# Kernel optimization log

Hardware: AMD Instinct MI355X
Metric: run time of the kernel (lower is better)

The kernel has to match this reference:

```python
import jax, jax.numpy as jnp
import numpy as np

C = 192
NUM_HEADS = 4
K = 3
KV_STRIDE = 2
EPS = 1e-5


def _conv(x, w, stride, groups):
    # x: [B,C,H,W], w: [O, I//groups, kh, kw]
    return jax.lax.conv_general_dilated(
        x, w, window_strides=(stride, stride),
        padding=[(K // 2, K // 2), (K // 2, K // 2)] if w.shape[-1] > 1 else [(0, 0), (0, 0)],
        dimension_numbers=("NCHW", "OIHW", "NCHW"),
        feature_group_count=groups)


def _bn(x, gamma, beta, mean, var):
    # eval-mode batchnorm over channel dim of NCHW
    inv = gamma / jnp.sqrt(var + EPS)
    return x * inv[None, :, None, None] + (beta - mean * inv)[None, :, None, None]


def _dwconv_flatten(x, dw, g, b, m, v, pw, stride):
    y = _conv(x, dw, stride, groups=C)          # depthwise
    y = _bn(y, g, b, m, v)
    y = _conv(y, pw, 1, groups=1)               # 1x1 pointwise
    B, O, h, w = y.shape
    return y.reshape(B, O, h * w).transpose(0, 2, 1)  # b (h w) c


def setup_inputs() -> dict:
    key = jax.random.key(0)
    ks = jax.random.split(key, 16)
    B, H, W = 8, 56, 56
    d = {
        "x": jax.random.normal(ks[0], (B, H * W, C), jnp.float32),
        "H": H,
        "W": W,
        "dw_q": jax.random.normal(ks[1], (C, 1, K, K), jnp.float32) * 0.1,
        "bn_q_gamma": jax.random.uniform(ks[2], (C,), jnp.float32, 0.5, 1.5),
        "bn_q_beta": jax.random.normal(ks[3], (C,), jnp.float32) * 0.1,
        "bn_q_mean": jax.random.normal(ks[4], (C,), jnp.float32) * 0.1,
        "bn_q_var": jax.random.uniform(ks[5], (C,), jnp.float32, 0.5, 1.5),
        "pw_q": jax.random.normal(ks[6], (C, C, 1, 1), jnp.float32) * (1.0 / np.sqrt(C)),
        "dw_kv": jax.random.normal(ks[7], (C, 1, K, K), jnp.float32) * 0.1,
        "bn_kv_gamma": jax.random.uniform(ks[8], (C,), jnp.float32, 0.5, 1.5),
        "bn_kv_beta": jax.random.normal(ks[9], (C,), jnp.float32) * 0.1,
        "bn_kv_mean": jax.random.normal(ks[10], (C,), jnp.float32) * 0.1,
        "bn_kv_var": jax.random.uniform(ks[11], (C,), jnp.float32, 0.5, 1.5),
        "pw_kv": jax.random.normal(ks[12], (2 * C, C, 1, 1), jnp.float32) * (1.0 / np.sqrt(C)),
        "Wq": jax.random.normal(ks[13], (C, C), jnp.float32) * (1.0 / np.sqrt(C)),
        "bq": jnp.zeros((C,), jnp.float32),
        "Wk": jax.random.normal(ks[14], (C, C), jnp.float32) * (1.0 / np.sqrt(C)),
        "bk": jnp.zeros((C,), jnp.float32),
        "Wv": jax.random.normal(ks[15], (C, C), jnp.float32) * (1.0 / np.sqrt(C)),
        "bv": jnp.zeros((C,), jnp.float32),
    }
    return d


def reference(x, H, W, dw_q, bn_q_gamma, bn_q_beta, bn_q_mean, bn_q_var, pw_q,
              dw_kv, bn_kv_gamma, bn_kv_beta, bn_kv_mean, bn_kv_var, pw_kv,
              Wq, bq, Wk, bk, Wv, bv):
    B, N, _ = x.shape
    h = NUM_HEADS
    hd = C // h
    scale = hd ** -0.5
    # Token2Patch: b (H W) c -> b c H W
    xp = x.transpose(0, 2, 1).reshape(B, C, H, W)
    conv_q = _dwconv_flatten(xp, dw_q, bn_q_gamma, bn_q_beta, bn_q_mean, bn_q_var, pw_q, 1)  # [B,N,C]
    kv = _dwconv_flatten(xp, dw_kv, bn_kv_gamma, bn_kv_beta, bn_kv_mean, bn_kv_var, pw_kv, KV_STRIDE)  # [B,M,2C]
    conv_k, conv_v = kv[..., :C], kv[..., C:]
    q = (conv_q @ Wq.T + bq).reshape(B, N, h, hd).transpose(0, 2, 1, 3)      # [B,h,N,hd]
    M = conv_k.shape[1]
    k = (conv_k @ Wk.T + bk).reshape(B, M, h, hd).transpose(0, 2, 1, 3)      # [B,h,M,hd]
    v = (conv_v @ Wv.T + bv).reshape(B, M, h, hd).transpose(0, 2, 1, 3)      # [B,h,M,hd]
    attn = jnp.einsum("bhnd,bhmd->bhnm", q, k) * scale
    attn = jax.nn.softmax(attn, axis=-1)
    out = jnp.einsum("bhnm,bhmd->bhnd", attn, v)
    # MergeHeads: b h n d -> b n (h d)
    return out.transpose(0, 2, 1, 3).reshape(B, N, C)
```

## Files before the change

kernel.cpp:

```cpp
#include <hip/hip_runtime.h>
#include <cmath>

typedef _Float16 f16;
typedef _Float16 f16x8 __attribute__((ext_vector_type(8)));
typedef _Float16 f16x4 __attribute__((ext_vector_type(4)));
typedef float    f32x4 __attribute__((ext_vector_type(4)));
typedef unsigned int u32;
typedef u32 u32x2 __attribute__((ext_vector_type(2)));

#define C_   192
#define HH   56
#define WW   56
#define NN   3136
#define BB   8
#define MM   784
#define NHEAD 4
#define HD   48
#define VT_LD 832
#define KVPB (BB*MM/32)

#define MFMA16(a,b,c)  __builtin_amdgcn_mfma_f32_16x16x32_f16(a,b,c,0,0,0)
#define MFMAK16(a,b,c) __builtin_amdgcn_mfma_f32_16x16x16f16(a,b,c,0,0,0)

static __device__ __forceinline__ u32 pkrtz(float a, float b) {
    typedef __fp16 fp16x2 __attribute__((ext_vector_type(2)));
    fp16x2 h = __builtin_amdgcn_cvt_pkrtz(a, b);
    return __builtin_bit_cast(u32, h);
}

static __device__ __forceinline__ void gload16(const void* g, void* l) {
    __builtin_amdgcn_global_load_lds(
        (const __attribute__((address_space(1))) unsigned int*)g,
        (__attribute__((address_space(3))) unsigned int*)l, 16, 0, 0);
}

template<int STRIDE, int OH, int OW>
__device__ __forceinline__ void dwbn_quad(
    const float* __restrict__ x, const float* __restrict__ dwL,
    const float* __restrict__ gamma, const float* __restrict__ beta,
    const float* __restrict__ mean,  const float* __restrict__ var,
    f16* __restrict__ out, int idx)
{
    int c4 = idx % 48;
    int r1 = idx / 48;
    int qx = r1 % (OW/2);
    int r2 = r1 / (OW/2);
    int qp = r2 % (OH/2);
    int b  = r2 / (OH/2);
    int c0 = c4*4;

    float4 w4[9];
    #pragma unroll
    for (int j = 0; j < 9; ++j)
        w4[j] = *(const float4*)&dwL[c4*40 + j*4];
    const float* wf = (const float*)w4;

    float4 g4  = *(const float4*)(gamma + c0);
    float4 be4 = *(const float4*)(beta + c0);
    float4 m4  = *(const float4*)(mean + c0);
    float4 v4  = *(const float4*)(var  + c0);

    float4 a00 = make_float4(0.f,0.f,0.f,0.f);
    float4 a01 = a00, a10 = a00, a11 = a00;
    int iyTop = (2*qp)*STRIDE - 1;
    int ix0   = (2*qx)*STRIDE - 1;
    #pragma unroll
    for (int j = 0; j < STRIDE+3; ++j) {
        int iy = iyTop + j;
        if (iy < 0 || iy >= HH) continue;
        #pragma unroll
        for (int i = 0; i < STRIDE+3; ++i) {
            int ix = ix0 + i;
            if (ix < 0 || ix >= WW) continue;
            float4 xv = *reinterpret_cast<const float4*>(
                x + ((size_t)b*NN + iy*WW + ix)*C_ + c0);
            const bool r0ok = (j <= 2), r1ok = (j >= STRIDE);
            const bool c0ok = (i <= 2), c1ok = (i >= STRIDE);
            if (r0ok && c0ok) { const int wi = j*3 + i;
                a00.x = fmaf(wf[ 0+wi], xv.x, a00.x);
                a00.y = fmaf(wf[ 9+wi], xv.y, a00.y);
                a00.z = fmaf(wf[18+wi], xv.z, a00.z);
                a00.w = fmaf(wf[27+wi], xv.w, a00.w); }
            if (r0ok && c1ok) { const int wi = j*3 + (i-STRIDE);
                a01.x = fmaf(wf[ 0+wi], xv.x, a01.x);
                a01.y = fmaf(wf[ 9+wi], xv.y, a01.y);
                a01.z = fmaf(wf[18+wi], xv.z, a01.z);
                a01.w = fmaf(wf[27+wi], xv.w, a01.w); }
            if (r1ok && c0ok) { const int wi = (j-STRIDE)*3 + i;
                a10.x = fmaf(wf[ 0+wi], xv.x, a10.x);
                a10.y = fmaf(wf[ 9+wi], xv.y, a10.y);
                a10.z = fmaf(wf[18+wi], xv.z, a10.z);
                a10.w = fmaf(wf[27+wi], xv.w, a10.w); }
            if (r1ok && c1ok) { const int wi = (j-STRIDE)*3 + (i-STRIDE);
                a11.x = fmaf(wf[ 0+wi], xv.x, a11.x);
                a11.y = fmaf(wf[ 9+wi], xv.y, a11.y);
                a11.z = fmaf(wf[18+wi], xv.z, a11.z);
                a11.w = fmaf(wf[27+wi], xv.w, a11.w); }
        }
    }
    float i0 = g4.x*__frsqrt_rn(v4.x + 1e-5f);
    float i1 = g4.y*__frsqrt_rn(v4.y + 1e-5f);
    float i2 = g4.z*__frsqrt_rn(v4.z + 1e-5f);
    float i3 = g4.w*__frsqrt_rn(v4.w + 1e-5f);
    float b0 = be4.x - m4.x*i0, b1 = be4.y - m4.y*i1;
    float b2 = be4.z - m4.z*i2, b3 = be4.w - m4.w*i3;
    size_t base = (((size_t)b*OH + 2*qp)*OW + 2*qx)*48 + c4;
    f16x4 r;
    r[0]=(f16)(a00.x*i0+b0); r[1]=(f16)(a00.y*i1+b1);
    r[2]=(f16)(a00.z*i2+b2); r[3]=(f16)(a00.w*i3+b3);
    *reinterpret_cast<f16x4*>(out + base*4) = r;
    r[0]=(f16)(a01.x*i0+b0); r[1]=(f16)(a01.y*i1+b1);
    r[2]=(f16)(a01.z*i2+b2); r[3]=(f16)(a01.w*i3+b3);
    *reinterpret_cast<f16x4*>(out + (base + 48)*4) = r;
    r[0]=(f16)(a10.x*i0+b0); r[1]=(f16)(a10.y*i1+b1);
    r[2]=(f16)(a10.z*i2+b2); r[3]=(f16)(a10.w*i3+b3);
    *reinterpret_cast<f16x4*>(out + (base + (size_t)OW*48)*4) = r;
    r[0]=(f16)(a11.x*i0+b0); r[1]=(f16)(a11.y*i1+b1);
    r[2]=(f16)(a11.z*i2+b2); r[3]=(f16)(a11.w*i3+b3);
    *reinterpret_cast<f16x4*>(out + (base + (size_t)OW*48 + 48)*4) = r;
}

__global__ __launch_bounds__(256) void prep_all(
    const float* __restrict__ x,
    const float* __restrict__ dwq,  const float* __restrict__ gq,
    const float* __restrict__ bq_,  const float* __restrict__ mq,
    const float* __restrict__ vq,
    const float* __restrict__ dwkv, const float* __restrict__ gkv,
    const float* __restrict__ bkv,  const float* __restrict__ mkv,
    const float* __restrict__ vkv,
    const float* __restrict__ Wq, const float* __restrict__ Wk,
    const float* __restrict__ Wv, const float* __restrict__ pw_q,
    const float* __restrict__ pw_kv,
    f16* __restrict__ uq, f16* __restrict__ ukv,
    f16* __restrict__ Mq, f16* __restrict__ Mk, f16* __restrict__ Mv,
    f16* __restrict__ vt)
{
    int blk = blockIdx.x, tid = threadIdx.x;
    const int QB = 1176, KB = 294;
    if (blk < QB + KB) {
        bool qp = blk < QB;
        __shared__ __align__(16) float dwL[48*40];
        const float* dwg = qp ? dwq : dwkv;
        for (int i = tid; i < 432; i += 256) {
            int f  = i*4;
            int c4 = f/36, r = f%36;
            *(float4*)&dwL[c4*40 + r] = *(const float4*)(dwg + f);
        }
        __syncthreads();
        if (qp)
            dwbn_quad<1, HH, WW>(x, dwL, gq, bq_, mq, vq, uq, blk*256 + tid);
        else
            dwbn_quad<2, 28, 28>(x, dwL, gkv, bkv, mkv, vkv, ukv,
                                 (blk - QB)*256 + tid);
    } else if (blk < QB + KB + 576) {
        int fb = blk - QB - KB;
        int which = fb / 192, o = fb % 192;
        const float* Wm = which == 0 ? Wq : (which == 1 ? Wk : Wv);
        const float* P  = which == 0 ? pw_q : (which == 1 ? pw_kv : pw_kv + C_*C_);
        f16* Mo         = which == 0 ? Mq : (which == 1 ? Mk : Mv);
        __shared__ float wrow[C_];
        if (tid < C_) wrow[tid] = Wm[o*C_ + tid];
        __syncthreads();
        if (tid < C_) {
            float acc = 0.f;
            #pragma unroll 8
            for (int j = 0; j < C_; ++j)
                acc = fmaf(wrow[j], P[j*C_ + tid], acc);
            Mo[o*C_ + tid] = (f16)acc;
        }
    } else {
        int i = (blk - QB - KB - 576)*256 + tid;
        int b = i / (C_*48);
        int rem = i % (C_*48);
        int c = rem / 48;
        int m = MM + (rem % 48);
        vt[((size_t)b*C_ + c)*VT_LD + m] = (f16)0.f;
    }
}

__global__ __launch_bounds__(128, 1) void proj_kv(
    const f16* __restrict__ ukv,
    const f16* __restrict__ Mk, const f16* __restrict__ Mv,
    const float* __restrict__ bk, const float* __restrict__ bv,
    f16* __restrict__ kb, f16* __restrict__ vt)
{
    int tid  = threadIdx.x;
    int w    = tid >> 6, l = tid & 63;
    int lrow = l & 15,  lgrp = l >> 4;
    int blk  = blockIdx.x;
    int path = blk < KVPB ? 1 : 2;
    int rblk = path == 1 ? blk : blk - KVPB;
    int r0 = rblk*32 + w*16;

    const f16* urow = ukv + (size_t)(r0 + lrow)*C_;
    f16x8 a[6];
    #pragma unroll
    for (int ch = 0; ch < 6; ++ch)
        a[ch] = *(const f16x8*)(urow + ch*32 + lgrp*8);

    f16x8 bfA[6], bfB[6];
    const f16* Mm = path == 1 ? Mk : Mv;

    #pragma unroll
    for (int ch = 0; ch < 6; ++ch)
        bfA[ch] = *(const f16x8*)(Mm + (size_t)lrow*C_ + ch*32 + lgrp*8);

    if (path == 1) {
        #pragma unroll
        for (int ct = 0; ct < 12; ++ct) {
            f16x8* cur = (ct & 1) ? bfB : bfA;
            f16x8* nxt = (ct & 1) ? bfA : bfB;
            if (ct < 11) {
                const f16* mrow = Mm + (size_t)((ct+1)*16 + lrow)*C_;
                #pragma unroll
                for (int ch = 0; ch < 6; ++ch)
                    nxt[ch] = *(const f16x8*)(mrow + ch*32 + lgrp*8);
            }
            f32x4 acc = {0.f,0.f,0.f,0.f};
            #pragma unroll
            for (int ch = 0; ch < 6; ++ch)
                acc = MFMA16(cur[ch], a[ch], acc);
            float4 bo = *(const float4*)(bk + ct*16 + lgrp*4);
            f16x4 st;
            st[0] = (f16)(acc[0] + bo.x);
            st[1] = (f16)(acc[1] + bo.y);
            st[2] = (f16)(acc[2] + bo.z);
            st[3] = (f16)(acc[3] + bo.w);
            *(f16x4*)(kb + (size_t)(r0 + lrow)*C_ + ct*16 + lgrp*4) = st;
        }
    } else {
        #pragma unroll
        for (int ct = 0; ct < 12; ++ct) {
            f16x8* cur = (ct & 1) ? bfB : bfA;
            f16x8* nxt = (ct & 1) ? bfA : bfB;
            if (ct < 11) {
                const f16* mrow = Mv + (size_t)((ct+1)*16 + lrow)*C_;
                #pragma unroll
                for (int ch = 0; ch < 6; ++ch)
                    nxt[ch] = *(const f16x8*)(mrow + ch*32 + lgrp*8);
            }
            int o = ct*16 + lrow;
            f32x4 acc = {0.f,0.f,0.f,0.f};
            #pragma unroll
            for (int ch = 0; ch < 6; ++ch)
                acc = MFMA16(a[ch], cur[ch], acc);
            float bo = bv[o];
            int rg = r0 + lgrp*4;
            int b  = rg / MM, m = rg % MM;
            f16x4 st;
            st[0] = (f16)(acc[0] + bo);
            st[1] = (f16)(acc[1] + bo);
            st[2] = (f16)(acc[2] + bo);
            st[3] = (f16)(acc[3] + bo);
            *(f16x4*)(vt + ((size_t)b*C_ + o)*VT_LD + m) = st;
        }
    }
}

__device__ __forceinline__ void stage_tile(
    int w, int l, f16* ldsKb, f16* ldsVb,
    const f16* __restrict__ kbb, const f16* __restrict__ vbb, int m0)
{
    int rr = l >> 3, p = l & 7;
    #pragma unroll
    for (int j = 0; j < 4; ++j) {
        int u = w + j*4;
        if (u < 8) {
            int r = u*8 + rr;
            int c = p ^ (r & 7);
            gload16(kbb + (size_t)(m0 + r)*C_ + c*8, ldsKb + u*512);
        } else if (u < 14) {
            int d = (u-8)*8 + rr;
            int c = p ^ (d & 7);
            gload16(vbb + (size_t)d*VT_LD + m0 + c*8, ldsVb + (u-8)*512);
        }
    }
}

__device__ __forceinline__ float softmax_upd(
    f32x4* s, float& mrun, float& lrun, u32* pk)
{
    float t0 = fmaxf(fmaxf(s[0][0], s[0][1]), fmaxf(s[0][2], s[0][3]));
    float t1 = fmaxf(fmaxf(s[1][0], s[1][1]), fmaxf(s[1][2], s[1][3]));
    float t2 = fmaxf(fmaxf(s[2][0], s[2][1]), fmaxf(s[2][2], s[2][3]));
    float t3 = fmaxf(fmaxf(s[3][0], s[3][1]), fmaxf(s[3][2], s[3][3]));
    float tmax = fmaxf(fmaxf(t0, t1), fmaxf(t2, t3));
    tmax = fmaxf(tmax, __shfl_xor(tmax, 16));
    tmax = fmaxf(tmax, __shfl_xor(tmax, 32));
    float mnew = fmaxf(mrun, tmax);
    float corr = exp2f(mrun - mnew);
    mrun = mnew;
    float psum = 0.f;
    #pragma unroll
    for (int j = 0; j < 4; ++j) {
        #pragma unroll
        for (int r = 0; r < 4; ++r) {
            s[j][r] = exp2f(s[j][r] - mnew);
            psum += s[j][r];
        }
    }
    lrun = lrun*corr + psum;
    #pragma unroll
    for (int j = 0; j < 4; ++j) {
        pk[j*2]   = pkrtz(s[j][0], s[j][1]);
        pk[j*2+1] = pkrtz(s[j][2], s[j][3]);
    }
    return corr;
}

__device__ __forceinline__ void compute_tile64(
    const f16* ldsKb, const f16* ldsVb,
    const f16x8& qf0, const f16x4& qfh,
    float& mrun, float& lrun, f32x4& o0, f32x4& o1, f32x4& o2,
    int lrow, int g, bool tail)
{
    const char* kP = (const char*)ldsKb;
    const char* vP = (const char*)ldsVb;
    f32x4 z = {0.f,0.f,0.f,0.f};
    int sw = lrow & 7;
    int cA = (g ^ sw) << 4;
    int cH = (((4 + (g >> 1)) ^ sw) << 4) + ((g & 1) << 3);

    f32x4 s[4];
    __builtin_amdgcn_s_setprio(1);
    #pragma unroll
    for (int j = 0; j < 4; ++j) {
        const char* rb = kP + (16*j + lrow)*128;
        f32x4 t = MFMA16(*(const f16x8*)(rb + cA), qf0, z);
        s[j] = MFMAK16(*(const f16x4*)(rb + cH), qfh, t);
    }
    __builtin_amdgcn_s_setprio(0);

    if (tail) {
        f32x4 neg = {-1e30f,-1e30f,-1e30f,-1e30f};
        s[1] = neg; s[2] = neg; s[3] = neg;
    }

    u32 pk[8];
    float corr = softmax_upd(s, mrun, lrun, pk);

    #pragma unroll
    for (int r = 0; r < 4; ++r) { o0[r] *= corr; o1[r] *= corr; o2[r] *= corr; }

    #pragma unroll
    for (int ch = 0; ch < 4; ++ch) {
        u32x2 pw = { pk[2*ch], pk[2*ch+1] };
        f16x4 pb = __builtin_bit_cast(f16x4, pw);
        int off = (((2*ch + (g >> 1)) ^ sw) << 4) + ((g & 1) << 3);
        f16x4 v0 = *(const f16x4*)(vP + lrow*128      + off);
        f16x4 v1 = *(const f16x4*)(vP + (16+lrow)*128 + off);
        f16x4 v2 = *(const f16x4*)(vP + (32+lrow)*128 + off);
        __builtin_amdgcn_s_setprio(1);
        o0 = MFMAK16(v0, pb, o0);
        o1 = MFMAK16(v1, pb, o1);
        o2 = MFMAK16(v2, pb, o2);
        __builtin_amdgcn_s_setprio(0);
    }
}

__global__ __launch_bounds__(256, 2) void attn_mfma(
    const f16* __restrict__ uq, const f16* __restrict__ Mq,
    const float* __restrict__ bq,
    const f16* __restrict__ kb, const f16* __restrict__ vt,
    float* __restrict__ out)
{
    __shared__ __align__(16) f16 ldsK[2][64*64];
    __shared__ __align__(16) f16 ldsV[2][48*64];
    __shared__ __align__(16) f16 qL[4][16*56];

    int tid  = threadIdx.x;
    int w    = tid >> 6, l = tid & 63;
    int lrow = l & 15,  g = l >> 4;
    int swz  = (blockIdx.x & 7)*196 + (blockIdx.x >> 3);
    int bh   = swz / 49, qblk = swz % 49;
    int h    = bh & 3, b = bh >> 2;
    int n0   = qblk*64 + w*16;

    const f16* kbb = kb + (size_t)b*MM*C_ + h*HD;
    const f16* vbb = vt + ((size_t)b*C_ + h*HD)*VT_LD;

    stage_tile(w, l, &ldsK[0][0], &ldsV[0][0], kbb, vbb, 0);

    {
        const float qsc = 0.14433756729740643f * 1.4426950408889634f;
        f16* qw = &qL[w][0];
        const f16* urow = uq + ((size_t)b*NN + n0 + lrow)*C_;
        f16x8 ufr[6];
        #pragma unroll
        for (int ch = 0; ch < 6; ++ch)
            ufr[ch] = *(const f16x8*)(urow + ch*32 + g*8);
        #pragma unroll
        for (int dt = 0; dt < 3; ++dt) {
            const f16* mrow = Mq + (size_t)(h*HD + dt*16 + lrow)*C_;
            f32x4 acc = {0.f,0.f,0.f,0.f};
            #pragma unroll
            for (int ch = 0; ch < 6; ++ch)
                acc = MFMA16(*(const f16x8*)(mrow + ch*32 + g*8), ufr[ch], acc);
            float4 bo = *(const float4*)(bq + h*HD + dt*16 + g*4);
            f16x4 st;
            st[0] = (f16)((acc[0] + bo.x)*qsc);
            st[1] = (f16)((acc[1] + bo.y)*qsc);
            st[2] = (f16)((acc[2] + bo.z)*qsc);
            st[3] = (f16)((acc[3] + bo.w)*qsc);
            *(f16x4*)(qw + lrow*56 + dt*16 + g*4) = st;
        }
    }
    f16x8 qf0 = *(const f16x8*)(&qL[w][0] + lrow*56 + g*8);
    f16x4 qfh = *(const f16x4*)(&qL[w][0] + lrow*56 + 32 + g*4);
    asm volatile("" :: "v"(qf0), "v"(qfh));

    float mrun = -1e30f, lrun = 0.f;
    f32x4 o0 = {0.f,0.f,0.f,0.f}, o1 = o0, o2 = o0;

    for (int t = 0; t < 13; ++t) {
        int nb = t & 1;
        if (t < 12)
            stage_tile(w, l, &ldsK[nb^1][0], &ldsV[nb^1][0], kbb, vbb, (t+1)*64);
        __builtin_amdgcn_sched_barrier(0);
        if (t < 12) {
            if (w < 2) asm volatile("s_waitcnt vmcnt(4)" ::: "memory");
            else       asm volatile("s_waitcnt vmcnt(3)" ::: "memory");
        } else {
            asm volatile("s_waitcnt vmcnt(0)" ::: "memory");
        }
        __builtin_amdgcn_s_barrier();
        __builtin_amdgcn_sched_barrier(0);
        compute_tile64(&ldsK[nb][0], &ldsV[nb][0], qf0, qfh,
                       mrun, lrun, o0, o1, o2, lrow, g, t == 12);
        __builtin_amdgcn_sched_barrier(0);
        __builtin_amdgcn_s_barrier();
    }

    lrun += __shfl_xor(lrun, 16);
    lrun += __shfl_xor(lrun, 32);
    float inv = 1.f / lrun;
    f32x4 r0, r1, r2;
    #pragma unroll
    for (int r = 0; r < 4; ++r) {
        r0[r] = o0[r]*inv; r1[r] = o1[r]*inv; r2[r] = o2[r]*inv;
    }
    float* obase = out + ((size_t)b*NN + n0 + lrow)*C_ + h*HD + g*4;
    *(f32x4*)(obase)      = r0;
    *(f32x4*)(obase + 16) = r1;
    *(f32x4*)(obase + 32) = r2;
}

extern "C" void kernel_launch(void* const* d_in, const int* in_sizes, int n_in,
                              void* d_out, int out_size, void* d_ws, size_t ws_size,
                              hipStream_t stream)
{
    const float* x     = (const float*)d_in[0];
    const float* dw_q  = (const float*)d_in[3];
    const float* bnqg  = (const float*)d_in[4];
    const float* bnqb  = (const float*)d_in[5];
    const float* bnqm  = (const float*)d_in[6];
    const float* bnqv  = (const float*)d_in[7];
    const float* pw_q  = (const float*)d_in[8];
    const float* dw_kv = (const float*)d_in[9];
    const float* bnkg  = (const float*)d_in[10];
    const float* bnkb  = (const float*)d_in[11];
    const float* bnkm  = (const float*)d_in[12];
    const float* bnkvv = (const float*)d_in[13];
    const float* pw_kv = (const float*)d_in[14];
    const float* Wq    = (const float*)d_in[15];
    const float* bq    = (const float*)d_in[16];
    const float* Wk    = (const float*)d_in[17];
    const float* bk    = (const float*)d_in[18];
    const float* Wv    = (const float*)d_in[19];
    const float* bv    = (const float*)d_in[20];
    float* out = (float*)d_out;

    f16* p   = (f16*)d_ws;
    f16* Mq16  = p;  p += C_*C_;
    f16* Mk16  = p;  p += C_*C_;
    f16* Mv16  = p;  p += C_*C_;
    f16* uq16  = p;  p += (size_t)BB*NN*C_ + 256;
    f16* ukv16 = p;  p += (size_t)BB*MM*C_;
    f16* kb16  = p;  p += (size_t)BB*MM*C_ + 16384;
    f16* vt16  = p;  p += (size_t)BB*C_*VT_LD;

    prep_all<<<2334, 256, 0, stream>>>(
        x, dw_q, bnqg, bnqb, bnqm, bnqv,
        dw_kv, bnkg, bnkb, bnkm, bnkvv,
        Wq, Wk, Wv, pw_q, pw_kv,
        uq16, ukv16, Mq16, Mk16, Mv16, vt16);

    proj_kv<<<2*KVPB, 128, 0, stream>>>(
        ukv16, Mk16, Mv16, bk, bv, kb16, vt16);

    attn_mfma<<<1568, 256, 0, stream>>>(uq16, Mq16, bq, kb16, vt16, out);
}
```

Measured before the change: 100.4 us.

## Compute 2x4 output tiles per thread in stride-1 depthwise conv

The stride-1 depthwise conv+BN for the Q path now has each thread produce a 2x4 block of outputs instead of 2x2. This reuses more of each loaded input across neighbouring outputs and halves the number of prep blocks for that path. Separately, the Q-row fragment loads in the attention kernel are moved ahead of the K/V tile staging so their latency can overlap. The cost is more accumulator registers per thread and fewer threads in flight.

Measured after the change: 97.80 us. -2.6%, faster.

```diff
diff --git a/kernel.cpp b/kernel.cpp
--- a/kernel.cpp
+++ b/kernel.cpp
@@ -34,13 +34,93 @@
         (__attribute__((address_space(3))) unsigned int*)l, 16, 0, 0);
 }
 
-template<int STRIDE, int OH, int OW>
-__device__ __forceinline__ void dwbn_quad(
+__device__ __forceinline__ void dwbn_oct(
     const float* __restrict__ x, const float* __restrict__ dwL,
     const float* __restrict__ gamma, const float* __restrict__ beta,
     const float* __restrict__ mean,  const float* __restrict__ var,
     f16* __restrict__ out, int idx)
 {
+    int c4 = idx % 48;
+    int r1 = idx / 48;
+    int qx = r1 % (WW/4);
+    int r2 = r1 / (WW/4);
+    int qp = r2 % (HH/2);
+    int b  = r2 / (HH/2);
+    int c0 = c4*4;
+
+    float4 w4[9];
+    #pragma unroll
+    for (int j = 0; j < 9; ++j)
+        w4[j] = *(const float4*)&dwL[c4*40 + j*4];
+    const float* wf = (const float*)w4;
+
+    float4 g4  = *(const float4*)(gamma + c0);
+    float4 be4 = *(const float4*)(beta + c0);
+    float4 m4  = *(const float4*)(mean + c0);
+    float4 v4  = *(const float4*)(var  + c0);
+
+    float4 acc[2][4];
+    #pragma unroll
+    for (int jj = 0; jj < 2; ++jj)
+        #pragma unroll
+        for (int ii = 0; ii < 4; ++ii)
+            acc[jj][ii] = make_float4(0.f,0.f,0.f,0.f);
+
+    int iyTop = 2*qp - 1;
+    int ix0   = 4*qx - 1;
+    #pragma unroll
+    for (int j = 0; j < 4; ++j) {
+        int iy = iyTop + j;
+        if (iy < 0 || iy >= HH) continue;
+        #pragma unroll
+        for (int i = 0; i < 6; ++i) {
+            int ix = ix0 + i;
+            if (ix < 0 || ix >= WW) continue;
+            float4 xv = *reinterpret_cast<const float4*>(
+                x + ((size_t)b*NN + iy*WW + ix)*C_ + c0);
+            #pragma unroll
+            for (int jj = 0; jj < 2; ++jj) {
+                if (j < jj || j > jj+2) continue;
+                #pragma unroll
+                for (int ii = 0; ii < 4; ++ii) {
+                    if (i < ii || i > ii+2) continue;
+                    const int wi = (j-jj)*3 + (i-ii);
+                    acc[jj][ii].x = fmaf(wf[ 0+wi], xv.x, acc[jj][ii].x);
+                    acc[jj][ii].y = fmaf(wf[ 9+wi], xv.y, acc[jj][ii].y);
+                    acc[jj][ii].z = fmaf(wf[18+wi], xv.z, acc[jj][ii].z);
+                    acc[jj][ii].w = fmaf(wf[27+wi], xv.w, acc[jj][ii].w);
+                }
+            }
+        }
+    }
+    float i0 = g4.x*__frsqrt_rn(v4.x + 1e-5f);
+    float i1 = g4.y*__frsqrt_rn(v4.y + 1e-5f);
+    float i2 = g4.z*__frsqrt_rn(v4.z + 1e-5f);
+    float i3 = g4.w*__frsqrt_rn(v4.w + 1e-5f);
+    float b0 = be4.x - m4.x*i0, b1 = be4.y - m4.y*i1;
+    float b2 = be4.z - m4.z*i2, b3 = be4.w - m4.w*i3;
+    #pragma unroll
+    for (int jj = 0; jj < 2; ++jj) {
+        #pragma unroll
+        for (int ii = 0; ii < 4; ++ii) {
+            f16x4 r;
+            r[0] = (f16)(acc[jj][ii].x*i0 + b0);
+            r[1] = (f16)(acc[jj][ii].y*i1 + b1);
+            r[2] = (f16)(acc[jj][ii].z*i2 + b2);
+            r[3] = (f16)(acc[jj][ii].w*i3 + b3);
+            size_t o = (((size_t)b*HH + 2*qp + jj)*WW + 4*qx + ii)*48 + c4;
+            *reinterpret_cast<f16x4*>(out + o*4) = r;
+        }
+    }
+}
+
+__device__ __forceinline__ void dwbn_quad2(
+    const float* __restrict__ x, const float* __restrict__ dwL,
+    const float* __restrict__ gamma, const float* __restrict__ beta,
+    const float* __restrict__ mean,  const float* __restrict__ var,
+    f16* __restrict__ out, int idx)
+{
+    const int OH = 28, OW = 28, STRIDE = 2;
     int c4 = idx % 48;
     int r1 = idx / 48;
     int qx = r1 % (OW/2);
@@ -136,7 +216,7 @@
     f16* __restrict__ vt)
 {
     int blk = blockIdx.x, tid = threadIdx.x;
-    const int QB = 1176, KB = 294;
+    const int QB = 588, KB = 294;
     if (blk < QB + KB) {
         bool qp = blk < QB;
         __shared__ __align__(16) float dwL[48*40];
@@ -148,10 +228,9 @@
         }
         __syncthreads();
         if (qp)
-            dwbn_quad<1, HH, WW>(x, dwL, gq, bq_, mq, vq, uq, blk*256 + tid);
+            dwbn_oct(x, dwL, gq, bq_, mq, vq, uq, blk*256 + tid);
         else
-            dwbn_quad<2, 28, 28>(x, dwL, gkv, bkv, mkv, vkv, ukv,
-                                 (blk - QB)*256 + tid);
+            dwbn_quad2(x, dwL, gkv, bkv, mkv, vkv, ukv, (blk - QB)*256 + tid);
     } else if (blk < QB + KB + 576) {
         int fb = blk - QB - KB;
         int which = fb / 192, o = fb % 192;
@@ -379,16 +458,17 @@
     const f16* kbb = kb + (size_t)b*MM*C_ + h*HD;
     const f16* vbb = vt + ((size_t)b*C_ + h*HD)*VT_LD;
 
+    const f16* urow = uq + ((size_t)b*NN + n0 + lrow)*C_;
+    f16x8 ufr[6];
+    #pragma unroll
+    for (int ch = 0; ch < 6; ++ch)
+        ufr[ch] = *(const f16x8*)(urow + ch*32 + g*8);
+
     stage_tile(w, l, &ldsK[0][0], &ldsV[0][0], kbb, vbb, 0);
 
     {
         const float qsc = 0.14433756729740643f * 1.4426950408889634f;
         f16* qw = &qL[w][0];
-        const f16* urow = uq + ((size_t)b*NN + n0 + lrow)*C_;
-        f16x8 ufr[6];
-        #pragma unroll
-        for (int ch = 0; ch < 6; ++ch)
-            ufr[ch] = *(const f16x8*)(urow + ch*32 + g*8);
         #pragma unroll
         for (int dt = 0; dt < 3; ++dt) {
             const f16* mrow = Mq + (size_t)(h*HD + dt*16 + lrow)*C_;
@@ -479,7 +559,7 @@
     f16* kb16  = p;  p += (size_t)BB*MM*C_ + 16384;
     f16* vt16  = p;  p += (size_t)BB*C_*VT_LD;
 
-    prep_all<<<2334, 256, 0, stream>>>(
+    prep_all<<<1746, 256, 0, stream>>>(
         x, dw_q, bnqg, bnqb, bnqm, bnqv,
         dw_kv, bnkg, bnkb, bnkm, bnkvv,
         Wq, Wk, Wv, pw_q, pw_kv,
```
